# Performance work log

Hardware: AMD Instinct MI355X
Metric: run time of the kernel (lower is better)

The kernel has to match this reference:

```python
import jax, jax.numpy as jnp
import numpy as np

B = 4096          # events
L = 524288        # total set points (avg 128 per event)
CIN = 16          # per-point feature size (set feature 'a')
DVEC = 32         # flat feature size (feature 'b')
PHI = [128, 128, 64]
MLP = [256, 128]
EPS = 1e-5        # BatchNorm1d eps


def setup_inputs() -> dict:
    key = jax.random.key(0)
    ks = jax.random.split(key, 10)
    def n(k, shape, scale=0.05):
        return jax.random.normal(k, shape, dtype=jnp.float32) * scale
    return {
        "x_a": jax.random.normal(ks[0], (1, CIN, L), dtype=jnp.float32),
        "x_b": jax.random.normal(ks[1], (B, DVEC), dtype=jnp.float32),
        # row 0 -> counts for set feature 'a'; row 1 ignored (Reshape branch)
        "sample_indices": jnp.full((2, B), L // B, dtype=jnp.int32),
        "W1": n(ks[2], (PHI[0], CIN)),  "b1": jnp.zeros((PHI[0],), jnp.float32),
        "W2": n(ks[3], (PHI[1], PHI[0])), "b2": jnp.zeros((PHI[1],), jnp.float32),
        "W3": n(ks[4], (PHI[2], PHI[1])), "b3": jnp.zeros((PHI[2],), jnp.float32),
        "Wm1": n(ks[5], (MLP[0], PHI[2] + DVEC)), "bm1": jnp.zeros((MLP[0],), jnp.float32),
        "g1": jnp.ones((MLP[0],), jnp.float32), "be1": jnp.zeros((MLP[0],), jnp.float32),
        "Wm2": n(ks[6], (MLP[1], MLP[0])), "bm2": jnp.zeros((MLP[1],), jnp.float32),
        "g2": jnp.ones((MLP[1],), jnp.float32), "be2": jnp.zeros((MLP[1],), jnp.float32),
        "Wm3": n(ks[7], (1, MLP[1])), "bm3": jnp.zeros((1,), jnp.float32),
    }


def _bn(x, g, b):
    # BatchNorm1d, training-mode batch stats, biased variance (torch semantics)
    mu = jnp.mean(x, axis=0)
    var = jnp.var(x, axis=0)
    return (x - mu) * jax.lax.rsqrt(var + EPS) * g + b


def reference(x_a, x_b, sample_indices,
              W1, b1, W2, b2, W3, b3,
              Wm1, bm1, g1, be1, Wm2, bm2, g2, be2, Wm3, bm3):
    counts = sample_indices[0].astype(jnp.int32)                       # [B]
    bounds = jnp.concatenate([jnp.zeros((1,), jnp.int32), jnp.cumsum(counts)])  # [B+1]

    # PhiNet: pointwise Conv1d stack (kernel size 1) on [CIN, L]
    h = x_a[0]
    h = jax.nn.relu(jnp.einsum('oc,cl->ol', W1, h) + b1[:, None])
    h = jax.nn.relu(jnp.einsum('oc,cl->ol', W2, h) + b2[:, None])
    h = jax.nn.relu(jnp.einsum('oc,cl->ol', W3, h) + b3[:, None])      # [64, L]

    # fused segment-mean: point p belongs to segment j iff bounds[j] <= p < bounds[j+1]
    seg = jnp.searchsorted(bounds, jnp.arange(h.shape[1], dtype=jnp.int32), side='right') - 1
    sums = jax.ops.segment_sum(h.T, seg, num_segments=counts.shape[0])  # [B, 64]
    means = sums / jnp.maximum(counts, 1).astype(jnp.float32)[:, None]

    # feature order: sorted keys -> ('a' set repr, 'b' flat)
    z = jnp.concatenate([means, x_b.reshape(-1, DVEC)], axis=1)        # [B, 96]

    z = jax.nn.relu(_bn(z @ Wm1.T + bm1, g1, be1))
    z = jax.nn.relu(_bn(z @ Wm2.T + bm2, g2, be2))
    return jax.nn.sigmoid(z @ Wm3.T + bm3)                             # [B, 1]
```

## Files before the change

kernel.cpp:

```cpp
#include <hip/hip_runtime.h>
#include <hip/hip_bf16.h>

#define B_EVENTS 4096
#define L_PTS    524288
#define CIN      16
#define C1       128
#define C2       128
#define C3       64
#define DVEC     32
#define ZDIM     96
#define M1       256
#define M2       128
#define BN_EPS   1e-5f
#define TPTS     64
#define EPB      2

typedef __attribute__((ext_vector_type(8))) short bf16x8;
typedef __attribute__((ext_vector_type(4))) float f32x4;

__device__ __forceinline__ ushort f2bf(float x) {
    union { float f; unsigned u; } a; a.f = x;
    unsigned r = (a.u + 0x7fffu + ((a.u >> 16) & 1u)) >> 16;
    return (ushort)r;
}

__device__ __forceinline__ unsigned cvtpk(float lo, float hi) {
    unsigned r;
    asm("v_cvt_pk_bf16_f32 %0, %1, %2" : "=v"(r) : "v"(lo), "v"(hi));
    return r;
}

__device__ __forceinline__ unsigned long long pack4relu(f32x4 a) {
    union { unsigned u[2]; unsigned long long ll; } pk;
    pk.u[0] = cvtpk(fmaxf(a[0], 0.f), fmaxf(a[1], 0.f));
    pk.u[1] = cvtpk(fmaxf(a[2], 0.f), fmaxf(a[3], 0.f));
    return pk.ll;
}

__device__ __forceinline__ int ldsoff(int base, int rowSlots, int c, int sir) {
    int s = c * rowSlots + sir;
    s ^= (c & 7);
    return base + s * 16;
}

__global__ __launch_bounds__(1024) void scanprep_kernel(
    const int* __restrict__ si, int* __restrict__ bounds, float* __restrict__ stats,
    const float* __restrict__ W1, const float* __restrict__ W2, const float* __restrict__ W3,
    ushort* __restrict__ w1p, ushort* __restrict__ w2b, ushort* __restrict__ w3b)
{
    if (blockIdx.x == 0) {
        __shared__ int sh[1024];
        const int tid = threadIdx.x;
        const int c0 = si[tid*4+0], c1 = si[tid*4+1], c2 = si[tid*4+2], c3 = si[tid*4+3];
        const int s4 = c0 + c1 + c2 + c3;
        sh[tid] = s4;
        if (tid < 768) stats[tid] = 0.f;
        __syncthreads();
        for (int off = 1; off < 1024; off <<= 1) {
            int add = (tid >= off) ? sh[tid - off] : 0;
            __syncthreads();
            sh[tid] += add;
            __syncthreads();
        }
        const int excl = (tid == 0) ? 0 : sh[tid - 1];
        bounds[tid*4+0] = excl;
        bounds[tid*4+1] = excl + c0;
        bounds[tid*4+2] = excl + c0 + c1;
        bounds[tid*4+3] = excl + c0 + c1 + c2;
        if (tid == 1023) bounds[B_EVENTS] = excl + s4;
    } else {
        const int tid = (blockIdx.x - 1) * 1024 + threadIdx.x;
        const int nthr = 4 * 1024;
        for (int i = tid; i < C1 * 32; i += nthr) {
            const int r = i >> 5, k = i & 31;
            w1p[i] = (k < CIN) ? f2bf(W1[r * CIN + k]) : (ushort)0;
        }
        for (int i = tid; i < C2 * C1; i += nthr) w2b[i] = f2bf(W2[i]);
        for (int i = tid; i < C3 * C2; i += nthr) w3b[i] = f2bf(W3[i]);
    }
}

__global__ __launch_bounds__(256, 2) void phi_mfma_kernel(
    const float* __restrict__ xa, const float* __restrict__ xb,
    const int* __restrict__ bounds,
    const ushort* __restrict__ w1p, const ushort* __restrict__ w2b, const ushort* __restrict__ w3b,
    const float* __restrict__ b1, const float* __restrict__ b2, const float* __restrict__ b3,
    float* __restrict__ z)
{
    __shared__ __align__(16) char lds[37376];

    const int tid  = threadIdx.x;
    const int lane = tid & 63;
    const int wid  = tid >> 6;
    const int wm   = wid >> 1;
    const int wn   = wid & 1;
    const int g4   = lane >> 4;
    const int c16  = lane & 15;

    bf16x8 a1[4], a2[4][4], a3[2][4];
    {
        const int r1 = wm * 64 + c16;
        #pragma unroll
        for (int mf = 0; mf < 4; ++mf)
            a1[mf] = *(const bf16x8*)&w1p[(r1 + mf * 16) * 32 + g4 * 8];
        #pragma unroll
        for (int mf = 0; mf < 4; ++mf)
            #pragma unroll
            for (int kf = 0; kf < 4; ++kf)
                a2[mf][kf] = *(const bf16x8*)&w2b[(r1 + mf * 16) * C1 + kf * 32 + g4 * 8];
        const int r3 = wm * 32 + c16;
        #pragma unroll
        for (int mf = 0; mf < 2; ++mf)
            #pragma unroll
            for (int kf = 0; kf < 4; ++kf)
                a3[mf][kf] = *(const bf16x8*)&w3b[(r3 + mf * 16) * C2 + kf * 32 + g4 * 8];
    }

    const int pt = tid & 63;
    const int q  = tid >> 6;
    const int xw = pt * 32 + q * 8;

    if (tid < 128)
        *(unsigned long long*)(lds + (tid >> 1) * 32 + 16 + (tid & 1) * 8) = 0ull;

    int j     = blockIdx.x * EPB;
    int start = bounds[j];
    int end   = bounds[j + 1];
    int cnt   = end - start;
    bool staged = false;

    for (int e = 0; e < EPB; ++e, ++j) {
        int end2 = 0, cnt2 = 0;
        if (e + 1 < EPB) { end2 = bounds[j + 2]; cnt2 = end2 - end; }

        if (!staged) {
            union { unsigned u[2]; unsigned long long ll; } pk;
            float v0 = (pt < cnt) ? xa[(size_t)(q * 4 + 0) * L_PTS + start + pt] : 0.f;
            float v1 = (pt < cnt) ? xa[(size_t)(q * 4 + 1) * L_PTS + start + pt] : 0.f;
            float v2 = (pt < cnt) ? xa[(size_t)(q * 4 + 2) * L_PTS + start + pt] : 0.f;
            float v3 = (pt < cnt) ? xa[(size_t)(q * 4 + 3) * L_PTS + start + pt] : 0.f;
            pk.u[0] = cvtpk(v0, v1);
            pk.u[1] = cvtpk(v2, v3);
            *(unsigned long long*)(lds + xw) = pk.ll;
            __syncthreads();
        }

        float s[2][4];
        #pragma unroll
        for (int mf = 0; mf < 2; ++mf)
            #pragma unroll
            for (int r = 0; r < 4; ++r) s[mf][r] = 0.f;

        for (int p0 = 0; p0 < cnt; p0 += TPTS) {
            const bool inEvt  = (p0 + TPTS) < cnt;
            const bool nxtEvt = !inEvt && (e + 1 < EPB);
            const bool pre    = inEvt || nxtEvt;

            float xr0 = 0.f, xr1 = 0.f, xr2 = 0.f, xr3 = 0.f;
            if (pre) {
                const int nbase = inEvt ? (start + p0 + TPTS) : end;
                const int nrem  = inEvt ? (cnt - p0 - TPTS) : cnt2;
                xr0 = (pt < nrem) ? xa[(size_t)(q * 4 + 0) * L_PTS + nbase + pt] : 0.f;
                xr1 = (pt < nrem) ? xa[(size_t)(q * 4 + 1) * L_PTS + nbase + pt] : 0.f;
                xr2 = (pt < nrem) ? xa[(size_t)(q * 4 + 2) * L_PTS + nbase + pt] : 0.f;
                xr3 = (pt < nrem) ? xa[(size_t)(q * 4 + 3) * L_PTS + nbase + pt] : 0.f;
            }

            {
                f32x4 acc[4][2];
                #pragma unroll
                for (int mf = 0; mf < 4; ++mf) {
                    const f32x4 bb = *(const f32x4*)&b1[wm * 64 + mf * 16 + g4 * 4];
                    acc[mf][0] = bb; acc[mf][1] = bb;
                }
                bf16x8 bfrag[2];
                #pragma unroll
                for (int nf = 0; nf < 2; ++nf)
                    bfrag[nf] = *(const bf16x8*)(lds + (wn * 32 + nf * 16 + c16) * 32 + g4 * 16);
                __builtin_amdgcn_s_setprio(1);
                #pragma unroll
                for (int nf = 0; nf < 2; ++nf)
                    #pragma unroll
                    for (int mf = 0; mf < 4; ++mf)
                        acc[mf][nf] = __builtin_amdgcn_mfma_f32_16x16x32_bf16(a1[mf], bfrag[nf], acc[mf][nf], 0, 0, 0);
                __builtin_amdgcn_s_setprio(0);
                #pragma unroll
                for (int mf = 0; mf < 4; ++mf)
                    #pragma unroll
                    for (int nf = 0; nf < 2; ++nf) {
                        const int c = wn * 32 + nf * 16 + c16;
                        const int sir = (wm * 64 + mf * 16) / 8 + (g4 >> 1);
                        *(unsigned long long*)(lds + ldsoff(4096, 16, c, sir) + (g4 & 1) * 8) = pack4relu(acc[mf][nf]);
                    }
            }
            __syncthreads();

            {
                f32x4 acc[4][2];
                #pragma unroll
                for (int mf = 0; mf < 4; ++mf) {
                    const f32x4 bb = *(const f32x4*)&b2[wm * 64 + mf * 16 + g4 * 4];
                    acc[mf][0] = bb; acc[mf][1] = bb;
                }
                #pragma unroll
                for (int nf = 0; nf < 2; ++nf) {
                    const int c = wn * 32 + nf * 16 + c16;
                    bf16x8 bk[4];
                    #pragma unroll
                    for (int kf = 0; kf < 4; ++kf)
                        bk[kf] = *(const bf16x8*)(lds + ldsoff(4096, 16, c, kf * 4 + g4));
                    __builtin_amdgcn_s_setprio(1);
                    #pragma unroll
                    for (int mf = 0; mf < 4; ++mf)
                        #pragma unroll
                        for (int kf = 0; kf < 4; ++kf)
                            acc[mf][nf] = __builtin_amdgcn_mfma_f32_16x16x32_bf16(a2[mf][kf], bk[kf], acc[mf][nf], 0, 0, 0);
                    __builtin_amdgcn_s_setprio(0);
                }
                if (pre) {
                    union { unsigned u[2]; unsigned long long ll; } pk;
                    pk.u[0] = cvtpk(xr0, xr1);
                    pk.u[1] = cvtpk(xr2, xr3);
                    *(unsigned long long*)(lds + xw) = pk.ll;
                }
                #pragma unroll
                for (int mf = 0; mf < 4; ++mf)
                    #pragma unroll
                    for (int nf = 0; nf < 2; ++nf) {
                        const int c = wn * 32 + nf * 16 + c16;
                        const int sir = (wm * 64 + mf * 16) / 8 + (g4 >> 1);
                        *(unsigned long long*)(lds + ldsoff(20480, 16, c, sir) + (g4 & 1) * 8) = pack4relu(acc[mf][nf]);
                    }
            }
            __syncthreads();

            {
                f32x4 acc3[2][2];
                #pragma unroll
                for (int mf = 0; mf < 2; ++mf) {
                    const f32x4 bb = *(const f32x4*)&b3[wm * 32 + mf * 16 + g4 * 4];
                    acc3[mf][0] = bb; acc3[mf][1] = bb;
                }
                #pragma unroll
                for (int nf = 0; nf < 2; ++nf) {
                    const int c = wn * 32 + nf * 16 + c16;
                    bf16x8 bk[4];
                    #pragma unroll
                    for (int kf = 0; kf < 4; ++kf)
                        bk[kf] = *(const bf16x8*)(lds + ldsoff(20480, 16, c, kf * 4 + g4));
                    __builtin_amdgcn_s_setprio(1);
                    #pragma unroll
                    for (int mf = 0; mf < 2; ++mf)
                        #pragma unroll
                        for (int kf = 0; kf < 4; ++kf)
                            acc3[mf][nf] = __builtin_amdgcn_mfma_f32_16x16x32_bf16(a3[mf][kf], bk[kf], acc3[mf][nf], 0, 0, 0);
                    __builtin_amdgcn_s_setprio(0);
                }
                #pragma unroll
                for (int nf = 0; nf < 2; ++nf) {
                    const int col = p0 + wn * 32 + nf * 16 + c16;
                    const bool valid = col < cnt;
                    #pragma unroll
                    for (int mf = 0; mf < 2; ++mf)
                        #pragma unroll
                        for (int r = 0; r < 4; ++r) {
                            const float v = fmaxf(acc3[mf][nf][r], 0.f);
                            if (valid) s[mf][r] += v;
                        }
                }
            }
        }

        #pragma unroll
        for (int mf = 0; mf < 2; ++mf)
            #pragma unroll
            for (int r = 0; r < 4; ++r) {
                float v = s[mf][r];
                v += __shfl_xor(v, 1, 64);
                v += __shfl_xor(v, 2, 64);
                v += __shfl_xor(v, 4, 64);
                v += __shfl_xor(v, 8, 64);
                if (c16 == 0)
                    *(float*)(lds + 36864 + (wn * 64 + wm * 32 + mf * 16 + g4 * 4 + r) * 4) = v;
            }
        __syncthreads();
        {
            const float inv = 1.f / (float)max(cnt, 1);
            if (tid < C3) {
                const float v = *(const float*)(lds + 36864 + tid * 4)
                              + *(const float*)(lds + 36864 + 256 + tid * 4);
                z[(size_t)j * ZDIM + tid] = v * inv;
            } else if (tid < ZDIM) {
                z[(size_t)j * ZDIM + tid] = xb[(size_t)j * DVEC + (tid - C3)];
            }
        }

        staged = (cnt > 0) && (e + 1 < EPB);
        if (e + 1 < EPB) { start = end; cnt = cnt2; end = end2; }
    }
}

__global__ __launch_bounds__(256) void mlp1_kernel(
    const float* __restrict__ z, const float* __restrict__ Wm1, const float* __restrict__ bm1,
    float* __restrict__ y1, float* __restrict__ gsum, float* __restrict__ gsq)
{
    __shared__ float zs[8][ZDIM + 4];
    const int r0 = blockIdx.x * 8;
    const int tid = threadIdx.x;
    for (int i = tid; i < 8 * ZDIM; i += 256) {
        const int r = i / ZDIM, c = i - r * ZDIM;
        zs[r][c] = z[(size_t)(r0 + r) * ZDIM + c];
    }
    __syncthreads();
    const int o = tid;
    float acc[8];
    const float bb = bm1[o];
    #pragma unroll
    for (int r = 0; r < 8; ++r) acc[r] = bb;
    for (int c = 0; c < ZDIM; c += 4) {
        const float4 w = *(const float4*)&Wm1[o * ZDIM + c];
        #pragma unroll
        for (int r = 0; r < 8; ++r) {
            const float4 v = *(const float4*)&zs[r][c];
            acc[r] += w.x*v.x + w.y*v.y + w.z*v.z + w.w*v.w;
        }
    }
    float s = 0.f, sq = 0.f;
    #pragma unroll
    for (int r = 0; r < 8; ++r) {
        y1[(size_t)(r0 + r) * M1 + o] = acc[r];
        s += acc[r]; sq += acc[r] * acc[r];
    }
    atomicAdd(&gsum[o], s);
    atomicAdd(&gsq[o], sq);
}

__global__ __launch_bounds__(256) void mlp2_kernel(
    const float* __restrict__ y1,
    const float* __restrict__ gsum1, const float* __restrict__ gsq1,
    const float* __restrict__ g1, const float* __restrict__ be1,
    const float* __restrict__ Wm2, const float* __restrict__ bm2,
    float* __restrict__ y2, float* __restrict__ gsum, float* __restrict__ gsq)
{
    __shared__ float zs[8][M1 + 4];
    __shared__ float sc[M1], sh[M1];
    const int r0 = blockIdx.x * 8;
    const int tid = threadIdx.x;
    {
        const float mu  = gsum1[tid] * (1.f / B_EVENTS);
        const float var = gsq1[tid] * (1.f / B_EVENTS) - mu * mu;
        const float s0  = rsqrtf(var + BN_EPS) * g1[tid];
        sc[tid] = s0;
        sh[tid] = be1[tid] - mu * s0;
    }
    __syncthreads();
    for (int i = tid; i < 8 * M1; i += 256) {
        const int r = i >> 8, c = i & (M1 - 1);
        const float v = y1[(size_t)(r0 + r) * M1 + c];
        zs[r][c] = fmaxf(v * sc[c] + sh[c], 0.f);
    }
    __syncthreads();
    const int o = tid & 127;
    const int h = tid >> 7;
    float acc[4];
    const float bb = bm2[o];
    #pragma unroll
    for (int r = 0; r < 4; ++r) acc[r] = bb;
    for (int c = 0; c < M1; c += 4) {
        const float4 w = *(const float4*)&Wm2[o * M1 + c];
        #pragma unroll
        for (int r = 0; r < 4; ++r) {
            const float4 v = *(const float4*)&zs[h * 4 + r][c];
            acc[r] += w.x*v.x + w.y*v.y + w.z*v.z + w.w*v.w;
        }
    }
    float s = 0.f, sq = 0.f;
    #pragma unroll
    for (int r = 0; r < 4; ++r) {
        y2[(size_t)(r0 + h * 4 + r) * M2 + o] = acc[r];
        s += acc[r]; sq += acc[r] * acc[r];
    }
    atomicAdd(&gsum[o], s);
    atomicAdd(&gsq[o], sq);
}

__global__ __launch_bounds__(256) void final_kernel(
    const float* __restrict__ y2,
    const float* __restrict__ gsum2, const float* __restrict__ gsq2,
    const float* __restrict__ g2, const float* __restrict__ be2,
    const float* __restrict__ Wm3, const float* __restrict__ bm3,
    float* __restrict__ out)
{
    __shared__ float sc[M2], sh[M2];
    const int tid = threadIdx.x;
    if (tid < M2) {
        const float mu  = gsum2[tid] * (1.f / B_EVENTS);
        const float var = gsq2[tid] * (1.f / B_EVENTS) - mu * mu;
        const float s0  = rsqrtf(var + BN_EPS) * g2[tid];
        sc[tid] = s0;
        sh[tid] = be2[tid] - mu * s0;
    }
    __syncthreads();
    const int w = tid >> 6, l = tid & 63;
    const int r = blockIdx.x * 4 + w;
    const float e0 = fmaxf(y2[(size_t)r * M2 + l]      * sc[l]      + sh[l],      0.f);
    const float e1 = fmaxf(y2[(size_t)r * M2 + 64 + l] * sc[64 + l] + sh[64 + l], 0.f);
    float a = e0 * Wm3[l] + e1 * Wm3[64 + l];
    #pragma unroll
    for (int off = 32; off >= 1; off >>= 1) a += __shfl_down(a, off, 64);
    if (l == 0) out[r] = 1.f / (1.f + expf(-(a + bm3[0])));
}

extern "C" void kernel_launch(void* const* d_in, const int* in_sizes, int n_in,
                              void* d_out, int out_size, void* d_ws, size_t ws_size,
                              hipStream_t stream) {
    const float* xa  = (const float*)d_in[0];
    const float* xb  = (const float*)d_in[1];
    const int*   si  = (const int*)  d_in[2];
    const float* W1  = (const float*)d_in[3];
    const float* b1  = (const float*)d_in[4];
    const float* W2  = (const float*)d_in[5];
    const float* b2  = (const float*)d_in[6];
    const float* W3  = (const float*)d_in[7];
    const float* b3  = (const float*)d_in[8];
    const float* Wm1 = (const float*)d_in[9];
    const float* bm1 = (const float*)d_in[10];
    const float* g1  = (const float*)d_in[11];
    const float* be1 = (const float*)d_in[12];
    const float* Wm2 = (const float*)d_in[13];
    const float* bm2 = (const float*)d_in[14];
    const float* g2  = (const float*)d_in[15];
    const float* be2 = (const float*)d_in[16];
    const float* Wm3 = (const float*)d_in[17];
    const float* bm3 = (const float*)d_in[18];
    float* out = (float*)d_out;

    char* ws = (char*)d_ws;
    size_t off = 0;
    auto alloc = [&](size_t bytes) -> void* {
        void* p = ws + off;
        off = (off + bytes + 255) & ~(size_t)255;
        return p;
    };
    int*    bounds = (int*)   alloc((B_EVENTS + 1) * sizeof(int));
    float*  stats  = (float*) alloc(768 * sizeof(float));
    float*  z      = (float*) alloc((size_t)B_EVENTS * ZDIM * sizeof(float));
    float*  y1     = (float*) alloc((size_t)B_EVENTS * M1 * sizeof(float));
    float*  y2     = (float*) alloc((size_t)B_EVENTS * M2 * sizeof(float));
    ushort* w1p    = (ushort*)alloc(C1 * 32 * sizeof(ushort));
    ushort* w2b    = (ushort*)alloc(C2 * C1 * sizeof(ushort));
    ushort* w3b    = (ushort*)alloc(C3 * C2 * sizeof(ushort));
    float* gsum1 = stats;
    float* gsq1  = stats + 256;
    float* gsum2 = stats + 512;
    float* gsq2  = stats + 640;

    hipLaunchKernelGGL(scanprep_kernel, dim3(5), dim3(1024), 0, stream,
                       si, bounds, stats, W1, W2, W3, w1p, w2b, w3b);
    hipLaunchKernelGGL(phi_mfma_kernel, dim3(B_EVENTS / EPB), dim3(256), 0, stream,
                       xa, xb, bounds, w1p, w2b, w3b, b1, b2, b3, z);
    hipLaunchKernelGGL(mlp1_kernel, dim3(B_EVENTS / 8), dim3(256), 0, stream,
                       z, Wm1, bm1, y1, gsum1, gsq1);
    hipLaunchKernelGGL(mlp2_kernel, dim3(B_EVENTS / 8), dim3(256), 0, stream,
                       y1, gsum1, gsq1, g1, be1, Wm2, bm2, y2, gsum2, gsq2);
    hipLaunchKernelGGL(final_kernel, dim3(B_EVENTS / 4), dim3(256), 0, stream,
                       y2, gsum2, gsq2, g2, be2, Wm3, bm3, out);
}
```

Before: 143.4 us.

## Fuse prefix-scan and weight conversion into phi kernel, raise events per block

Drops the separate scan/prep kernel. Each phi block now computes its own segment bounds by summing all counts before its first event, and converts W1/W2/W3 from fp32 to bf16 while loading them into registers. Biases move into LDS and are added at the ReLU/pack step instead of seeding the accumulators, and the events per block go from two to four. This saves one kernel launch and its dependency, but every block now repeats the prefix sum and the weight conversion. The LDS padding that used to be zeroed is no longer zeroed, so correctness relies on the zeroed A fragments masking whatever is left there.

```diff
diff --git a/kernel.cpp b/kernel.cpp
--- a/kernel.cpp
+++ b/kernel.cpp
@@ -13,16 +13,21 @@
 #define M2       128
 #define BN_EPS   1e-5f
 #define TPTS     64
-#define EPB      2
+#define EPB      4
+
+#define XOFF   0
+#define H1OFF  4096
+#define H2OFF  20480
+#define PART   36864
+#define BIAS1  37376
+#define BIAS2  37888
+#define BIAS3  38400
+#define SCR    38656
+#define SBND   38672
+#define LDSSZ  38720
 
 typedef __attribute__((ext_vector_type(8))) short bf16x8;
 typedef __attribute__((ext_vector_type(4))) float f32x4;
-
-__device__ __forceinline__ ushort f2bf(float x) {
-    union { float f; unsigned u; } a; a.f = x;
-    unsigned r = (a.u + 0x7fffu + ((a.u >> 16) & 1u)) >> 16;
-    return (ushort)r;
-}
 
 __device__ __forceinline__ unsigned cvtpk(float lo, float hi) {
     unsigned r;
@@ -30,11 +35,22 @@
     return r;
 }
 
-__device__ __forceinline__ unsigned long long pack4relu(f32x4 a) {
+__device__ __forceinline__ unsigned long long pack4relub(f32x4 a, f32x4 b) {
     union { unsigned u[2]; unsigned long long ll; } pk;
-    pk.u[0] = cvtpk(fmaxf(a[0], 0.f), fmaxf(a[1], 0.f));
-    pk.u[1] = cvtpk(fmaxf(a[2], 0.f), fmaxf(a[3], 0.f));
+    pk.u[0] = cvtpk(fmaxf(a[0] + b[0], 0.f), fmaxf(a[1] + b[1], 0.f));
+    pk.u[1] = cvtpk(fmaxf(a[2] + b[2], 0.f), fmaxf(a[3] + b[3], 0.f));
     return pk.ll;
+}
+
+__device__ __forceinline__ bf16x8 frag_from_f32(const float* p) {
+    const float4 lo = *(const float4*)p;
+    const float4 hi = *(const float4*)(p + 4);
+    union { unsigned u[4]; bf16x8 v; } r;
+    r.u[0] = cvtpk(lo.x, lo.y);
+    r.u[1] = cvtpk(lo.z, lo.w);
+    r.u[2] = cvtpk(hi.x, hi.y);
+    r.u[3] = cvtpk(hi.z, hi.w);
+    return r.v;
 }
 
 __device__ __forceinline__ int ldsoff(int base, int rowSlots, int c, int sir) {
@@ -43,51 +59,14 @@
     return base + s * 16;
 }
 
-__global__ __launch_bounds__(1024) void scanprep_kernel(
-    const int* __restrict__ si, int* __restrict__ bounds, float* __restrict__ stats,
-    const float* __restrict__ W1, const float* __restrict__ W2, const float* __restrict__ W3,
-    ushort* __restrict__ w1p, ushort* __restrict__ w2b, ushort* __restrict__ w3b)
-{
-    if (blockIdx.x == 0) {
-        __shared__ int sh[1024];
-        const int tid = threadIdx.x;
-        const int c0 = si[tid*4+0], c1 = si[tid*4+1], c2 = si[tid*4+2], c3 = si[tid*4+3];
-        const int s4 = c0 + c1 + c2 + c3;
-        sh[tid] = s4;
-        if (tid < 768) stats[tid] = 0.f;
-        __syncthreads();
-        for (int off = 1; off < 1024; off <<= 1) {
-            int add = (tid >= off) ? sh[tid - off] : 0;
-            __syncthreads();
-            sh[tid] += add;
-            __syncthreads();
-        }
-        const int excl = (tid == 0) ? 0 : sh[tid - 1];
-        bounds[tid*4+0] = excl;
-        bounds[tid*4+1] = excl + c0;
-        bounds[tid*4+2] = excl + c0 + c1;
-        bounds[tid*4+3] = excl + c0 + c1 + c2;
-        if (tid == 1023) bounds[B_EVENTS] = excl + s4;
-    } else {
-        const int tid = (blockIdx.x - 1) * 1024 + threadIdx.x;
-        const int nthr = 4 * 1024;
-        for (int i = tid; i < C1 * 32; i += nthr) {
-            const int r = i >> 5, k = i & 31;
-            w1p[i] = (k < CIN) ? f2bf(W1[r * CIN + k]) : (ushort)0;
-        }
-        for (int i = tid; i < C2 * C1; i += nthr) w2b[i] = f2bf(W2[i]);
-        for (int i = tid; i < C3 * C2; i += nthr) w3b[i] = f2bf(W3[i]);
-    }
-}
-
 __global__ __launch_bounds__(256, 2) void phi_mfma_kernel(
     const float* __restrict__ xa, const float* __restrict__ xb,
-    const int* __restrict__ bounds,
-    const ushort* __restrict__ w1p, const ushort* __restrict__ w2b, const ushort* __restrict__ w3b,
+    const int* __restrict__ si,
+    const float* __restrict__ W1, const float* __restrict__ W2, const float* __restrict__ W3,
     const float* __restrict__ b1, const float* __restrict__ b2, const float* __restrict__ b3,
-    float* __restrict__ z)
+    float* __restrict__ stats, float* __restrict__ z)
 {
-    __shared__ __align__(16) char lds[37376];
+    __shared__ __align__(16) char lds[LDSSZ];
 
     const int tid  = threadIdx.x;
     const int lane = tid & 63;
@@ -97,48 +76,75 @@
     const int g4   = lane >> 4;
     const int c16  = lane & 15;
 
+    if (blockIdx.x == 0)
+        for (int i = tid; i < 768; i += 256) stats[i] = 0.f;
+
+    if (tid < 128) {
+        ((float*)(lds + BIAS1))[tid] = b1[tid];
+        ((float*)(lds + BIAS2))[tid] = b2[tid];
+    } else if (tid < 192) {
+        ((float*)(lds + BIAS3))[tid - 128] = b3[tid - 128];
+    }
+
+    const int j0 = blockIdx.x * EPB;
+    {
+        int psum = 0;
+        for (int i = tid; i < j0; i += 256) psum += si[i];
+        #pragma unroll
+        for (int m = 1; m < 64; m <<= 1) psum += __shfl_xor(psum, m, 64);
+        if (lane == 0) ((int*)(lds + SCR))[wid] = psum;
+    }
+    __syncthreads();
+    if (tid == 0) {
+        const int* scr = (const int*)(lds + SCR);
+        int b = scr[0] + scr[1] + scr[2] + scr[3];
+        int* sb = (int*)(lds + SBND);
+        sb[0] = b;
+        #pragma unroll
+        for (int e = 0; e < EPB; ++e) { b += si[j0 + e]; sb[e + 1] = b; }
+    }
+
     bf16x8 a1[4], a2[4][4], a3[2][4];
     {
+        const bf16x8 zz = {0, 0, 0, 0, 0, 0, 0, 0};
         const int r1 = wm * 64 + c16;
         #pragma unroll
         for (int mf = 0; mf < 4; ++mf)
-            a1[mf] = *(const bf16x8*)&w1p[(r1 + mf * 16) * 32 + g4 * 8];
+            a1[mf] = (g4 < 2) ? frag_from_f32(&W1[(r1 + mf * 16) * CIN + g4 * 8]) : zz;
         #pragma unroll
         for (int mf = 0; mf < 4; ++mf)
             #pragma unroll
             for (int kf = 0; kf < 4; ++kf)
-                a2[mf][kf] = *(const bf16x8*)&w2b[(r1 + mf * 16) * C1 + kf * 32 + g4 * 8];
+                a2[mf][kf] = frag_from_f32(&W2[(r1 + mf * 16) * C1 + kf * 32 + g4 * 8]);
         const int r3 = wm * 32 + c16;
         #pragma unroll
         for (int mf = 0; mf < 2; ++mf)
             #pragma unroll
             for (int kf = 0; kf < 4; ++kf)
-                a3[mf][kf] = *(const bf16x8*)&w3b[(r3 + mf * 16) * C2 + kf * 32 + g4 * 8];
-    }
+                a3[mf][kf] = frag_from_f32(&W3[(r3 + mf * 16) * C2 + kf * 32 + g4 * 8]);
+    }
+    __syncthreads();
+    const int* sb = (const int*)(lds + SBND);
 
     const int pt = tid & 63;
     const int q  = tid >> 6;
     const int xw = pt * 32 + q * 8;
 
-    if (tid < 128)
-        *(unsigned long long*)(lds + (tid >> 1) * 32 + 16 + (tid & 1) * 8) = 0ull;
-
-    int j     = blockIdx.x * EPB;
-    int start = bounds[j];
-    int end   = bounds[j + 1];
-    int cnt   = end - start;
     bool staged = false;
 
-    for (int e = 0; e < EPB; ++e, ++j) {
-        int end2 = 0, cnt2 = 0;
-        if (e + 1 < EPB) { end2 = bounds[j + 2]; cnt2 = end2 - end; }
+    for (int e = 0; e < EPB; ++e) {
+        const int j     = j0 + e;
+        const int start = sb[e];
+        const int end   = sb[e + 1];
+        const int cnt   = end - start;
+        const int cnt2  = (e + 1 < EPB) ? sb[e + 2] - end : 0;
 
         if (!staged) {
             union { unsigned u[2]; unsigned long long ll; } pk;
-            float v0 = (pt < cnt) ? xa[(size_t)(q * 4 + 0) * L_PTS + start + pt] : 0.f;
-            float v1 = (pt < cnt) ? xa[(size_t)(q * 4 + 1) * L_PTS + start + pt] : 0.f;
-            float v2 = (pt < cnt) ? xa[(size_t)(q * 4 + 2) * L_PTS + start + pt] : 0.f;
-            float v3 = (pt < cnt) ? xa[(size_t)(q * 4 + 3) * L_PTS + start + pt] : 0.f;
+            const float v0 = (pt < cnt) ? xa[(size_t)(q * 4 + 0) * L_PTS + start + pt] : 0.f;
+            const float v1 = (pt < cnt) ? xa[(size_t)(q * 4 + 1) * L_PTS + start + pt] : 0.f;
+            const float v2 = (pt < cnt) ? xa[(size_t)(q * 4 + 2) * L_PTS + start + pt] : 0.f;
+            const float v3 = (pt < cnt) ? xa[(size_t)(q * 4 + 3) * L_PTS + start + pt] : 0.f;
             pk.u[0] = cvtpk(v0, v1);
             pk.u[1] = cvtpk(v2, v3);
             *(unsigned long long*)(lds + xw) = pk.ll;
@@ -170,8 +176,8 @@
                 f32x4 acc[4][2];
                 #pragma unroll
                 for (int mf = 0; mf < 4; ++mf) {
-                    const f32x4 bb = *(const f32x4*)&b1[wm * 64 + mf * 16 + g4 * 4];
-                    acc[mf][0] = bb; acc[mf][1] = bb;
+                    acc[mf][0] = f32x4{0.f, 0.f, 0.f, 0.f};
+                    acc[mf][1] = f32x4{0.f, 0.f, 0.f, 0.f};
                 }
                 bf16x8 bfrag[2];
                 #pragma unroll
@@ -185,13 +191,15 @@
                         acc[mf][nf] = __builtin_amdgcn_mfma_f32_16x16x32_bf16(a1[mf], bfrag[nf], acc[mf][nf], 0, 0, 0);
                 __builtin_amdgcn_s_setprio(0);
                 #pragma unroll
-                for (int mf = 0; mf < 4; ++mf)
+                for (int mf = 0; mf < 4; ++mf) {
+                    const f32x4 bb = *(const f32x4*)(lds + BIAS1 + (wm * 64 + mf * 16 + g4 * 4) * 4);
                     #pragma unroll
                     for (int nf = 0; nf < 2; ++nf) {
                         const int c = wn * 32 + nf * 16 + c16;
                         const int sir = (wm * 64 + mf * 16) / 8 + (g4 >> 1);
-                        *(unsigned long long*)(lds + ldsoff(4096, 16, c, sir) + (g4 & 1) * 8) = pack4relu(acc[mf][nf]);
+                        *(unsigned long long*)(lds + ldsoff(H1OFF, 16, c, sir) + (g4 & 1) * 8) = pack4relub(acc[mf][nf], bb);
                     }
+                }
             }
             __syncthreads();
 
@@ -199,8 +207,8 @@
                 f32x4 acc[4][2];
                 #pragma unroll
                 for (int mf = 0; mf < 4; ++mf) {
-                    const f32x4 bb = *(const f32x4*)&b2[wm * 64 + mf * 16 + g4 * 4];
-                    acc[mf][0] = bb; acc[mf][1] = bb;
+                    acc[mf][0] = f32x4{0.f, 0.f, 0.f, 0.f};
+                    acc[mf][1] = f32x4{0.f, 0.f, 0.f, 0.f};
                 }
                 #pragma unroll
                 for (int nf = 0; nf < 2; ++nf) {
@@ -208,7 +216,7 @@
                     bf16x8 bk[4];
                     #pragma unroll
                     for (int kf = 0; kf < 4; ++kf)
-                        bk[kf] = *(const bf16x8*)(lds + ldsoff(4096, 16, c, kf * 4 + g4));
+                        bk[kf] = *(const bf16x8*)(lds + ldsoff(H1OFF, 16, c, kf * 4 + g4));
                     __builtin_amdgcn_s_setprio(1);
                     #pragma unroll
                     for (int mf = 0; mf < 4; ++mf)
@@ -224,13 +232,15 @@
                     *(unsigned long long*)(lds + xw) = pk.ll;
                 }
                 #pragma unroll
-                for (int mf = 0; mf < 4; ++mf)
+                for (int mf = 0; mf < 4; ++mf) {
+                    const f32x4 bb = *(const f32x4*)(lds + BIAS2 + (wm * 64 + mf * 16 + g4 * 4) * 4);
                     #pragma unroll
                     for (int nf = 0; nf < 2; ++nf) {
                         const int c = wn * 32 + nf * 16 + c16;
                         const int sir = (wm * 64 + mf * 16) / 8 + (g4 >> 1);
-                        *(unsigned long long*)(lds + ldsoff(20480, 16, c, sir) + (g4 & 1) * 8) = pack4relu(acc[mf][nf]);
+                        *(unsigned long long*)(lds + ldsoff(H2OFF, 16, c, sir) + (g4 & 1) * 8) = pack4relub(acc[mf][nf], bb);
                     }
+                }
             }
             __syncthreads();
 
@@ -238,8 +248,8 @@
                 f32x4 acc3[2][2];
                 #pragma unroll
                 for (int mf = 0; mf < 2; ++mf) {
-                    const f32x4 bb = *(const f32x4*)&b3[wm * 32 + mf * 16 + g4 * 4];
-                    acc3[mf][0] = bb; acc3[mf][1] = bb;
+                    acc3[mf][0] = f32x4{0.f, 0.f, 0.f, 0.f};
+                    acc3[mf][1] = f32x4{0.f, 0.f, 0.f, 0.f};
                 }
                 #pragma unroll
                 for (int nf = 0; nf < 2; ++nf) {
@@ -247,7 +257,7 @@
                     bf16x8 bk[4];
                     #pragma unroll
                     for (int kf = 0; kf < 4; ++kf)
-                        bk[kf] = *(const bf16x8*)(lds + ldsoff(20480, 16, c, kf * 4 + g4));
+                        bk[kf] = *(const bf16x8*)(lds + ldsoff(H2OFF, 16, c, kf * 4 + g4));
                     __builtin_amdgcn_s_setprio(1);
                     #pragma unroll
                     for (int mf = 0; mf < 2; ++mf)
@@ -257,16 +267,18 @@
                     __builtin_amdgcn_s_setprio(0);
                 }
                 #pragma unroll
-                for (int nf = 0; nf < 2; ++nf) {
-                    const int col = p0 + wn * 32 + nf * 16 + c16;
-                    const bool valid = col < cnt;
-                    #pragma unroll
-                    for (int mf = 0; mf < 2; ++mf)
+                for (int mf = 0; mf < 2; ++mf) {
+                    const f32x4 bb = *(const f32x4*)(lds + BIAS3 + (wm * 32 + mf * 16 + g4 * 4) * 4);
+                    #pragma unroll
+                    for (int nf = 0; nf < 2; ++nf) {
+                        const int col = p0 + wn * 32 + nf * 16 + c16;
+                        const bool valid = col < cnt;
                         #pragma unroll
                         for (int r = 0; r < 4; ++r) {
-                            const float v = fmaxf(acc3[mf][nf][r], 0.f);
+                            const float v = fmaxf(acc3[mf][nf][r] + bb[r], 0.f);
                             if (valid) s[mf][r] += v;
                         }
+                    }
                 }
             }
         }
@@ -281,14 +293,14 @@
                 v += __shfl_xor(v, 4, 64);
                 v += __shfl_xor(v, 8, 64);
                 if (c16 == 0)
-                    *(float*)(lds + 36864 + (wn * 64 + wm * 32 + mf * 16 + g4 * 4 + r) * 4) = v;
+                    *(float*)(lds + PART + (wn * 64 + wm * 32 + mf * 16 + g4 * 4 + r) * 4) = v;
             }
         __syncthreads();
         {
             const float inv = 1.f / (float)max(cnt, 1);
             if (tid < C3) {
-                const float v = *(const float*)(lds + 36864 + tid * 4)
-                              + *(const float*)(lds + 36864 + 256 + tid * 4);
+                const float v = *(const float*)(lds + PART + tid * 4)
+                              + *(const float*)(lds + PART + 256 + tid * 4);
                 z[(size_t)j * ZDIM + tid] = v * inv;
             } else if (tid < ZDIM) {
                 z[(size_t)j * ZDIM + tid] = xb[(size_t)j * DVEC + (tid - C3)];
@@ -296,7 +308,6 @@
         }
 
         staged = (cnt > 0) && (e + 1 < EPB);
-        if (e + 1 < EPB) { start = end; cnt = cnt2; end = end2; }
     }
 }
 
@@ -442,23 +453,17 @@
         off = (off + bytes + 255) & ~(size_t)255;
         return p;
     };
-    int*    bounds = (int*)   alloc((B_EVENTS + 1) * sizeof(int));
-    float*  stats  = (float*) alloc(768 * sizeof(float));
-    float*  z      = (float*) alloc((size_t)B_EVENTS * ZDIM * sizeof(float));
-    float*  y1     = (float*) alloc((size_t)B_EVENTS * M1 * sizeof(float));
-    float*  y2     = (float*) alloc((size_t)B_EVENTS * M2 * sizeof(float));
-    ushort* w1p    = (ushort*)alloc(C1 * 32 * sizeof(ushort));
-    ushort* w2b    = (ushort*)alloc(C2 * C1 * sizeof(ushort));
-    ushort* w3b    = (ushort*)alloc(C3 * C2 * sizeof(ushort));
+    float* stats = (float*)alloc(768 * sizeof(float));
+    float* z     = (float*)alloc((size_t)B_EVENTS * ZDIM * sizeof(float));
+    float* y1    = (float*)alloc((size_t)B_EVENTS * M1 * sizeof(float));
+    float* y2    = (float*)alloc((size_t)B_EVENTS * M2 * sizeof(float));
     float* gsum1 = stats;
     float* gsq1  = stats + 256;
     float* gsum2 = stats + 512;
     float* gsq2  = stats + 640;
 
-    hipLaunchKernelGGL(scanprep_kernel, dim3(5), dim3(1024), 0, stream,
-                       si, bounds, stats, W1, W2, W3, w1p, w2b, w3b);
     hipLaunchKernelGGL(phi_mfma_kernel, dim3(B_EVENTS / EPB), dim3(256), 0, stream,
-                       xa, xb, bounds, w1p, w2b, w3b, b1, b2, b3, z);
+                       xa, xb, si, W1, W2, W3, b1, b2, b3, stats, z);
     hipLaunchKernelGGL(mlp1_kernel, dim3(B_EVENTS / 8), dim3(256), 0, stream,
                        z, Wm1, bm1, y1, gsum1, gsq1);
     hipLaunchKernelGGL(mlp2_kernel, dim3(B_EVENTS / 8), dim3(256), 0, stream,
```

After: 142.3 us. Within noise of the previous version (-0.8%).
